# Kernel tuning notes

Hardware: AMD Instinct MI355X
Metric: run time of the kernel (lower is better)

The kernel has to match this reference:

```python
import jax, jax.numpy as jnp
import numpy as np

EPS = float(np.finfo(np.float32).eps)
QMIN, QMAX = -128, 127


def setup_inputs() -> dict:
    key = jax.random.key(0)
    k_x, k_w, k_ws, k_b = jax.random.split(key, 4)
    M, K, N = 32768, 1024, 1024
    x = jax.random.normal(k_x, (M, K), dtype=jnp.float32)
    # per-channel symmetrically quantized, transposed weight: [K, N], values in [-128, 127]
    w_int8_t = jax.random.randint(k_w, (K, N), QMIN, QMAX + 1, dtype=jnp.int32).astype(jnp.int8)
    # per-out-channel scales (positive, float; torch uses float64, we use float32)
    w_scales = (jax.random.uniform(k_ws, (N,), dtype=jnp.float32) * 0.02 + 1e-4)
    # preprocessed column sums: w_int8_t.sum(dim=0)
    w_int8_t_sums = w_int8_t.astype(jnp.int32).sum(axis=0)
    bias = jax.random.normal(k_b, (N,), dtype=jnp.float32)
    return {
        "x": x,
        "w_int8_t": w_int8_t,
        "w_scales": w_scales,
        "w_int8_t_sums": w_int8_t_sums,
        "bias": bias,
    }


def reference(x, w_int8_t, w_scales, w_int8_t_sums, bias):
    # ---- dynamically_quantize_per_tensor (affine, int8) ----
    min_neg = jnp.minimum(jnp.min(x), jnp.float32(0.0))
    max_pos = jnp.maximum(jnp.max(x), jnp.float32(0.0))
    x_scale = jnp.maximum((max_pos - min_neg) / jnp.float32(QMAX - QMIN), EPS)
    x_zp = jnp.clip(QMIN - jnp.round(min_neg / x_scale), QMIN, QMAX)  # scalar
    x_q = jnp.clip(jnp.round(x / x_scale) + x_zp, QMIN, QMAX).astype(jnp.int8)

    # ---- int8 matmul with int32 accumulation (safe_int_mm equivalent) ----
    xw_i32 = jnp.matmul(
        x_q.astype(jnp.int32), w_int8_t.astype(jnp.int32)
    )  # [M, N] int32

    # ---- dequant with zero-point correction (quant_int8_matmul) ----
    mm_unscaled = xw_i32.astype(jnp.float32) - x_zp * w_int8_t_sums.astype(jnp.float32)
    y = x_scale * w_scales * mm_unscaled  # broadcast w_scales over N

    # ---- bias add (quant_int8_dynamic_linear) ----
    y = y + bias
    return y.astype(jnp.float32)
```

## Files before the change

### kernel.cpp

```cpp
#include <hip/hip_runtime.h>
#include <stdint.h>

#define M_DIM 32768
#define K_DIM 1024
#define N_DIM 1024

typedef int v4i __attribute__((ext_vector_type(4)));

__device__ __forceinline__ void gld_lds16(const void* g, void* lds) {
    __builtin_amdgcn_global_load_lds(
        (const __attribute__((address_space(1))) unsigned int*)g,
        (__attribute__((address_space(3))) unsigned int*)lds, 16, 0, 0);
}

__global__ void k_minmax(const float* __restrict__ x,
                         float* __restrict__ pmin, float* __restrict__ pmax) {
    int t = threadIdx.x;
    long gid = (long)blockIdx.x * blockDim.x + t;
    const float4* x4 = (const float4*)x;
    const long n4 = (long)M_DIM * K_DIM / 4;
    float mn = INFINITY, mx = -INFINITY;
    for (long i = gid; i < n4; i += (long)gridDim.x * blockDim.x) {
        float4 v = x4[i];
        mn = fminf(mn, fminf(fminf(v.x, v.y), fminf(v.z, v.w)));
        mx = fmaxf(mx, fmaxf(fmaxf(v.x, v.y), fmaxf(v.z, v.w)));
    }
    __shared__ float smn[256], smx[256];
    smn[t] = mn; smx[t] = mx;
    __syncthreads();
    for (int s = 128; s > 0; s >>= 1) {
        if (t < s) {
            smn[t] = fminf(smn[t], smn[t + s]);
            smx[t] = fmaxf(smx[t], smx[t + s]);
        }
        __syncthreads();
    }
    if (t == 0) { pmin[blockIdx.x] = smn[0]; pmax[blockIdx.x] = smx[0]; }
}

__global__ void k_finalize(const float* __restrict__ pmin,
                           const float* __restrict__ pmax,
                           float* __restrict__ sp) {
    int t = threadIdx.x;
    float mn = INFINITY, mx = -INFINITY;
    for (int i = t; i < 1024; i += 256) {
        mn = fminf(mn, pmin[i]);
        mx = fmaxf(mx, pmax[i]);
    }
    __shared__ float smn[256], smx[256];
    smn[t] = mn; smx[t] = mx;
    __syncthreads();
    for (int s = 128; s > 0; s >>= 1) {
        if (t < s) {
            smn[t] = fminf(smn[t], smn[t + s]);
            smx[t] = fmaxf(smx[t], smx[t + s]);
        }
        __syncthreads();
    }
    if (t == 0) {
        float min_neg = fminf(smn[0], 0.0f);
        float max_pos = fmaxf(smx[0], 0.0f);
        float scale = (max_pos - min_neg) / 255.0f;
        scale = fmaxf(scale, 1.1920928955078125e-07f);
        float zp = -128.0f - rintf(min_neg / scale);
        zp = fminf(fmaxf(zp, -128.0f), 127.0f);
        sp[0] = scale;
        sp[1] = zp;
    }
}

__device__ __forceinline__ unsigned q4(float4 v, float s, float zp) {
    int a = (int)fminf(fmaxf(rintf(v.x / s) + zp, -128.0f), 127.0f);
    int b = (int)fminf(fmaxf(rintf(v.y / s) + zp, -128.0f), 127.0f);
    int c = (int)fminf(fmaxf(rintf(v.z / s) + zp, -128.0f), 127.0f);
    int d = (int)fminf(fmaxf(rintf(v.w / s) + zp, -128.0f), 127.0f);
    return (a & 255) | ((b & 255) << 8) | ((c & 255) << 16) | ((d & 255) << 24);
}

__global__ void k_quant(const float* __restrict__ x,
                        const float* __restrict__ sp,
                        int8_t* __restrict__ xq) {
    float s = sp[0], zp = sp[1];
    long g = (long)blockIdx.x * blockDim.x + threadIdx.x;
    const float4* x4 = (const float4*)x + g * 4;
    float4 v0 = x4[0], v1 = x4[1], v2 = x4[2], v3 = x4[3];
    uint4 r;
    r.x = q4(v0, s, zp);
    r.y = q4(v1, s, zp);
    r.z = q4(v2, s, zp);
    r.w = q4(v3, s, zp);
    ((uint4*)xq)[g] = r;
}

__global__ void k_transpose(const int* __restrict__ w, int8_t* __restrict__ wt) {
    __shared__ int8_t tile[32][33];
    int bn = blockIdx.x * 32;
    int bk = blockIdx.y * 32;
    int tx = threadIdx.x, ty = threadIdx.y;
#pragma unroll
    for (int i = 0; i < 32; i += 8)
        tile[ty + i][tx] = (int8_t)w[(long)(bk + ty + i) * N_DIM + bn + tx];
    __syncthreads();
#pragma unroll
    for (int i = 0; i < 32; i += 8)
        wt[(long)(bn + ty + i) * K_DIM + bk + tx] = tile[tx][ty + i];
}

__global__ __launch_bounds__(256) void k_gemm(
    const int8_t* __restrict__ xq, const int8_t* __restrict__ wt,
    const float* __restrict__ sp, const float* __restrict__ w_scales,
    const int* __restrict__ wsums, const float* __restrict__ bias,
    float* __restrict__ out) {
    __shared__ __align__(16) int8_t lds_a[128 * 64];
    __shared__ __align__(16) int8_t lds_b[128 * 64];

    const int t = threadIdx.x;
    const int m0 = blockIdx.y * 128;
    const int n0 = blockIdx.x * 128;
    const int w = t >> 6, l = t & 63, quad = l >> 4, r = l & 15;
    const int wave_m = (w & 1) * 64, wave_n = (w >> 1) * 64;

    v4i acc[4][4];
#pragma unroll
    for (int i = 0; i < 4; i++)
#pragma unroll
        for (int j = 0; j < 4; j++) acc[i][j] = (v4i){0, 0, 0, 0};

    const int slot0 = t, slot1 = 256 + t;
    const int row0 = slot0 >> 2, s0 = slot0 & 3;
    const int row1 = slot1 >> 2, s1 = slot1 & 3;
    const int q0 = s0 ^ (row0 & 3) ^ ((row0 >> 2) & 3);
    const int q1 = s1 ^ (row1 & 3) ^ ((row1 >> 2) & 3);
    const int8_t* gA0 = xq + (long)(m0 + row0) * K_DIM + q0 * 16;
    const int8_t* gA1 = xq + (long)(m0 + row1) * K_DIM + q1 * 16;
    const int8_t* gB0 = wt + (long)(n0 + row0) * K_DIM + q0 * 16;
    const int8_t* gB1 = wt + (long)(n0 + row1) * K_DIM + q1 * 16;

    int ra[4], rb[4];
#pragma unroll
    for (int i = 0; i < 4; i++) {
        int mrow = wave_m + i * 16 + r;
        int sa = quad ^ (mrow & 3) ^ ((mrow >> 2) & 3);
        ra[i] = mrow * 64 + sa * 16;
        int nrow = wave_n + i * 16 + r;
        int sb = quad ^ (nrow & 3) ^ ((nrow >> 2) & 3);
        rb[i] = nrow * 64 + sb * 16;
    }

    for (int kb = 0; kb < K_DIM; kb += 64) {
        gld_lds16(gA0 + kb, lds_a + slot0 * 16);
        gld_lds16(gA1 + kb, lds_a + slot1 * 16);
        gld_lds16(gB0 + kb, lds_b + slot0 * 16);
        gld_lds16(gB1 + kb, lds_b + slot1 * 16);
        __syncthreads();

        v4i af[4], bf[4];
#pragma unroll
        for (int i = 0; i < 4; i++) af[i] = *(const v4i*)(lds_a + ra[i]);
#pragma unroll
        for (int j = 0; j < 4; j++) bf[j] = *(const v4i*)(lds_b + rb[j]);
#pragma unroll
        for (int i = 0; i < 4; i++)
#pragma unroll
            for (int j = 0; j < 4; j++)
                acc[i][j] = __builtin_amdgcn_mfma_i32_16x16x64_i8(af[i], bf[j], acc[i][j], 0, 0, 0);
        __syncthreads();
    }

    const float scale = sp[0], zp = sp[1];
#pragma unroll
    for (int j = 0; j < 4; j++) {
        int n = n0 + wave_n + j * 16 + r;
        float sj = scale * w_scales[n];
        float cj = zp * (float)wsums[n];
        float bj = bias[n];
#pragma unroll
        for (int i = 0; i < 4; i++) {
            int mbase = m0 + wave_m + i * 16 + quad * 4;
#pragma unroll
            for (int e = 0; e < 4; e++) {
                out[(long)(mbase + e) * N_DIM + n] = sj * ((float)acc[i][j][e] - cj) + bj;
            }
        }
    }
}

extern "C" void kernel_launch(void* const* d_in, const int* in_sizes, int n_in,
                              void* d_out, int out_size, void* d_ws, size_t ws_size,
                              hipStream_t stream) {
    const float* x        = (const float*)d_in[0];
    const int*   w_int8_t = (const int*)d_in[1];
    const float* w_scales = (const float*)d_in[2];
    const int*   w_sums   = (const int*)d_in[3];
    const float* bias     = (const float*)d_in[4];
    float* out = (float*)d_out;

    float* wsf  = (float*)d_ws;
    float* pmin = wsf;
    float* pmax = wsf + 1024;
    float* sp   = wsf + 2048;
    int8_t* wt  = (int8_t*)d_ws + 16384;
    int8_t* xq  = (int8_t*)d_ws + 16384 + (size_t)K_DIM * N_DIM;

    k_minmax<<<1024, 256, 0, stream>>>(x, pmin, pmax);
    k_finalize<<<1, 256, 0, stream>>>(pmin, pmax, sp);
    k_quant<<<8192, 256, 0, stream>>>(x, sp, xq);
    k_transpose<<<dim3(N_DIM / 32, K_DIM / 32), dim3(32, 8), 0, stream>>>(w_int8_t, wt);
    k_gemm<<<dim3(N_DIM / 128, M_DIM / 128), 256, 0, stream>>>(
        xq, wt, sp, w_scales, w_sums, bias, out);
}
```

Before: 318.5 us.

## Double-buffer GEMM LDS staging, swizzle block order, fuse transpose into minmax

Stages the next K tile into a second LDS buffer with asynchronous global-to-LDS loads while MFMAs consume the current one, removing one barrier per iteration. Remaps the 1D GEMM grid with a swizzle to change which output tiles run concurrently for cache reuse. Merges the weight transpose into the min/max reduction launch and makes the quantize kernel's loads and stores coalesced. Doubles GEMM LDS use, which may reduce occupancy.

```diff
diff --git a/kernel.cpp b/kernel.cpp
--- a/kernel.cpp
+++ b/kernel.cpp
@@ -13,29 +13,46 @@
         (__attribute__((address_space(3))) unsigned int*)lds, 16, 0, 0);
 }
 
-__global__ void k_minmax(const float* __restrict__ x,
-                         float* __restrict__ pmin, float* __restrict__ pmax) {
+__global__ void k_prep(const float* __restrict__ x,
+                       float* __restrict__ pmin, float* __restrict__ pmax,
+                       const int* __restrict__ w, int8_t* __restrict__ wt) {
     int t = threadIdx.x;
-    long gid = (long)blockIdx.x * blockDim.x + t;
-    const float4* x4 = (const float4*)x;
-    const long n4 = (long)M_DIM * K_DIM / 4;
-    float mn = INFINITY, mx = -INFINITY;
-    for (long i = gid; i < n4; i += (long)gridDim.x * blockDim.x) {
-        float4 v = x4[i];
-        mn = fminf(mn, fminf(fminf(v.x, v.y), fminf(v.z, v.w)));
-        mx = fmaxf(mx, fmaxf(fmaxf(v.x, v.y), fmaxf(v.z, v.w)));
-    }
-    __shared__ float smn[256], smx[256];
-    smn[t] = mn; smx[t] = mx;
-    __syncthreads();
-    for (int s = 128; s > 0; s >>= 1) {
-        if (t < s) {
-            smn[t] = fminf(smn[t], smn[t + s]);
-            smx[t] = fmaxf(smx[t], smx[t + s]);
-        }
-        __syncthreads();
-    }
-    if (t == 0) { pmin[blockIdx.x] = smn[0]; pmax[blockIdx.x] = smx[0]; }
+    if (blockIdx.x < 1024) {
+        long gid = (long)blockIdx.x * 256 + t;
+        const float4* x4 = (const float4*)x;
+        const long n4 = (long)M_DIM * K_DIM / 4;
+        float mn = INFINITY, mx = -INFINITY;
+#pragma unroll 4
+        for (long i = gid; i < n4; i += 1024 * 256) {
+            float4 v = x4[i];
+            mn = fminf(mn, fminf(fminf(v.x, v.y), fminf(v.z, v.w)));
+            mx = fmaxf(mx, fmaxf(fmaxf(v.x, v.y), fmaxf(v.z, v.w)));
+        }
+        __shared__ float smn[256], smx[256];
+        smn[t] = mn; smx[t] = mx;
+        __syncthreads();
+        for (int s = 128; s > 0; s >>= 1) {
+            if (t < s) {
+                smn[t] = fminf(smn[t], smn[t + s]);
+                smx[t] = fmaxf(smx[t], smx[t + s]);
+            }
+            __syncthreads();
+        }
+        if (t == 0) { pmin[blockIdx.x] = smn[0]; pmax[blockIdx.x] = smx[0]; }
+    } else {
+        __shared__ int8_t tile[32][33];
+        int b = blockIdx.x - 1024;
+        int bn = (b & 31) * 32;
+        int bk = (b >> 5) * 32;
+        int tx = t & 31, ty = t >> 5;
+#pragma unroll
+        for (int i = 0; i < 32; i += 8)
+            tile[ty + i][tx] = (int8_t)w[(long)(bk + ty + i) * N_DIM + bn + tx];
+        __syncthreads();
+#pragma unroll
+        for (int i = 0; i < 32; i += 8)
+            wt[(long)(bn + ty + i) * K_DIM + bk + tx] = tile[tx][ty + i];
+    }
 }
 
 __global__ void k_finalize(const float* __restrict__ pmin,
@@ -81,29 +98,16 @@
                         const float* __restrict__ sp,
                         int8_t* __restrict__ xq) {
     float s = sp[0], zp = sp[1];
-    long g = (long)blockIdx.x * blockDim.x + threadIdx.x;
-    const float4* x4 = (const float4*)x + g * 4;
-    float4 v0 = x4[0], v1 = x4[1], v2 = x4[2], v3 = x4[3];
-    uint4 r;
-    r.x = q4(v0, s, zp);
-    r.y = q4(v1, s, zp);
-    r.z = q4(v2, s, zp);
-    r.w = q4(v3, s, zp);
-    ((uint4*)xq)[g] = r;
-}
-
-__global__ void k_transpose(const int* __restrict__ w, int8_t* __restrict__ wt) {
-    __shared__ int8_t tile[32][33];
-    int bn = blockIdx.x * 32;
-    int bk = blockIdx.y * 32;
-    int tx = threadIdx.x, ty = threadIdx.y;
-#pragma unroll
-    for (int i = 0; i < 32; i += 8)
-        tile[ty + i][tx] = (int8_t)w[(long)(bk + ty + i) * N_DIM + bn + tx];
-    __syncthreads();
-#pragma unroll
-    for (int i = 0; i < 32; i += 8)
-        wt[(long)(bn + ty + i) * K_DIM + bk + tx] = tile[tx][ty + i];
+    const float4* x4 = (const float4*)x;
+    unsigned* q4out = (unsigned*)xq;
+    long base = (long)blockIdx.x * 1024;
+    int t = threadIdx.x;
+#pragma unroll
+    for (int v = 0; v < 4; v++) {
+        long i = base + (long)v * 256 + t;
+        float4 val = x4[i];
+        q4out[i] = q4(val, s, zp);
+    }
 }
 
 __global__ __launch_bounds__(256) void k_gemm(
@@ -111,12 +115,14 @@
     const float* __restrict__ sp, const float* __restrict__ w_scales,
     const int* __restrict__ wsums, const float* __restrict__ bias,
     float* __restrict__ out) {
-    __shared__ __align__(16) int8_t lds_a[128 * 64];
-    __shared__ __align__(16) int8_t lds_b[128 * 64];
+    __shared__ __align__(16) int8_t lds_a[2][128 * 64];
+    __shared__ __align__(16) int8_t lds_b[2][128 * 64];
 
     const int t = threadIdx.x;
-    const int m0 = blockIdx.y * 128;
-    const int n0 = blockIdx.x * 128;
+    const int orig = blockIdx.x;
+    const int swz = (orig & 7) * 256 + (orig >> 3);
+    const int m0 = (swz >> 3) * 128;
+    const int n0 = (swz & 7) * 128;
     const int w = t >> 6, l = t & 63, quad = l >> 4, r = l & 15;
     const int wave_m = (w & 1) * 64, wave_n = (w >> 1) * 64;
 
@@ -136,6 +142,14 @@
     const int8_t* gB0 = wt + (long)(n0 + row0) * K_DIM + q0 * 16;
     const int8_t* gB1 = wt + (long)(n0 + row1) * K_DIM + q1 * 16;
 
+#define STAGE(buf, kb)                                        \
+    do {                                                      \
+        gld_lds16(gA0 + (kb), lds_a[buf] + slot0 * 16);       \
+        gld_lds16(gA1 + (kb), lds_a[buf] + slot1 * 16);       \
+        gld_lds16(gB0 + (kb), lds_b[buf] + slot0 * 16);       \
+        gld_lds16(gB1 + (kb), lds_b[buf] + slot1 * 16);       \
+    } while (0)
+
     int ra[4], rb[4];
 #pragma unroll
     for (int i = 0; i < 4; i++) {
@@ -147,25 +161,28 @@
         rb[i] = nrow * 64 + sb * 16;
     }
 
-    for (int kb = 0; kb < K_DIM; kb += 64) {
-        gld_lds16(gA0 + kb, lds_a + slot0 * 16);
-        gld_lds16(gA1 + kb, lds_a + slot1 * 16);
-        gld_lds16(gB0 + kb, lds_b + slot0 * 16);
-        gld_lds16(gB1 + kb, lds_b + slot1 * 16);
-        __syncthreads();
+    STAGE(0, 0);
+    __syncthreads();
+
+    int cur = 0;
+    for (int kb = 64; kb <= K_DIM; kb += 64) {
+        if (kb < K_DIM) STAGE(cur ^ 1, kb);
 
         v4i af[4], bf[4];
 #pragma unroll
-        for (int i = 0; i < 4; i++) af[i] = *(const v4i*)(lds_a + ra[i]);
-#pragma unroll
-        for (int j = 0; j < 4; j++) bf[j] = *(const v4i*)(lds_b + rb[j]);
+        for (int i = 0; i < 4; i++) af[i] = *(const v4i*)(lds_a[cur] + ra[i]);
+#pragma unroll
+        for (int j = 0; j < 4; j++) bf[j] = *(const v4i*)(lds_b[cur] + rb[j]);
 #pragma unroll
         for (int i = 0; i < 4; i++)
 #pragma unroll
             for (int j = 0; j < 4; j++)
                 acc[i][j] = __builtin_amdgcn_mfma_i32_16x16x64_i8(af[i], bf[j], acc[i][j], 0, 0, 0);
-        __syncthreads();
-    }
+
+        __syncthreads();
+        cur ^= 1;
+    }
+#undef STAGE
 
     const float scale = sp[0], zp = sp[1];
 #pragma unroll
@@ -202,10 +219,8 @@
     int8_t* wt  = (int8_t*)d_ws + 16384;
     int8_t* xq  = (int8_t*)d_ws + 16384 + (size_t)K_DIM * N_DIM;
 
-    k_minmax<<<1024, 256, 0, stream>>>(x, pmin, pmax);
+    k_prep<<<2048, 256, 0, stream>>>(x, pmin, pmax, w_int8_t, wt);
     k_finalize<<<1, 256, 0, stream>>>(pmin, pmax, sp);
     k_quant<<<8192, 256, 0, stream>>>(x, sp, xq);
-    k_transpose<<<dim3(N_DIM / 32, K_DIM / 32), dim3(32, 8), 0, stream>>>(w_int8_t, wt);
-    k_gemm<<<dim3(N_DIM / 128, M_DIM / 128), 256, 0, stream>>>(
-        xq, wt, sp, w_scales, w_sums, bias, out);
-}
+    k_gemm<<<2048, 256, 0, stream>>>(xq, wt, sp, w_scales, w_sums, bias, out);
+}
```

Measured after the change: 320.7 us. No clear change (+0.7%).
